# Kernel optimization log

Measured on AMD Instinct MI355X. Metric: run time of the kernel, lower is better.

The kernel has to match this reference:

```python
import jax, jax.numpy as jnp
import numpy as np

N_NODES = 100000
N_EDGES = 1600000
N_GRAPHS = 1000
X_S = 128
HID = 64


def setup_inputs() -> dict:
    key = jax.random.key(0)
    ks = jax.random.split(key, 12)
    x = jax.random.normal(ks[0], (N_NODES, X_S), dtype=jnp.float32)
    edge_index = jax.random.randint(ks[1], (2, N_EDGES), 0, N_NODES, dtype=jnp.int64)
    batch = jnp.sort(jax.random.randint(ks[2], (N_NODES,), 0, N_GRAPHS, dtype=jnp.int64))
    def lin(k, fin, fout):
        s = 1.0 / np.sqrt(fin)
        kw, kb = jax.random.split(k)
        W = jax.random.uniform(kw, (fin, fout), minval=-s, maxval=s, dtype=jnp.float32)
        b = jax.random.uniform(kb, (fout,), minval=-s, maxval=s, dtype=jnp.float32)
        return W, b
    W1, b1 = lin(ks[3], X_S, HID)
    W2, b2 = lin(ks[4], HID, HID)
    W3, b3 = lin(ks[5], HID, HID)
    Wf, bf = lin(ks[6], HID, 10)
    Wl, bl = lin(ks[7], 10, 1)
    eps1 = jnp.float32(0.37)
    eps2 = jnp.float32(0.72)
    eps3 = jnp.float32(0.11)
    return {"x": x, "edge_index": edge_index, "batch": batch,
            "W1": W1, "b1": b1, "W2": W2, "b2": b2, "W3": W3, "b3": b3,
            "Wf": Wf, "bf": bf, "Wl": Wl, "bl": bl,
            "eps1": eps1, "eps2": eps2, "eps3": eps3}


def _gin_conv(h, src, dst, eps, W, b):
    # GIN: nn((1+eps)*x_i + sum_{j in N(i)} x_j); messages flow src -> dst
    agg = jax.ops.segment_sum(h[src], dst, num_segments=N_NODES)  # [N, d]
    return ((1.0 + eps) * h + agg) @ W + b


def reference(x, edge_index, batch, W1, b1, W2, b2, W3, b3, Wf, bf, Wl, bl,
              eps1, eps2, eps3):
    src, dst = edge_index[0], edge_index[1]
    h = jax.nn.relu(_gin_conv(x, src, dst, eps1, W1, b1))
    h = jax.nn.relu(_gin_conv(h, src, dst, eps2, W2, b2))
    h = jax.nn.relu(_gin_conv(h, src, dst, eps3, W3, b3))
    # global_mean_pool over graph ids
    sums = jax.ops.segment_sum(h, batch, num_segments=N_GRAPHS)        # [G, 64]
    cnts = jax.ops.segment_sum(jnp.ones((N_NODES,), h.dtype), batch,
                               num_segments=N_GRAPHS)                   # [G]
    pooled = sums / jnp.maximum(cnts, 1.0)[:, None]
    out = jax.nn.relu(pooled @ Wf + bf) @ Wl + bl                       # [G, 1]
    return out
```

## Files before the change

kernel.cpp:

```cpp
#include <hip/hip_runtime.h>

#define N_NODES 100000
#define N_EDGES 1600000
#define N_GRAPHS 1000

#define NB_C 782
#define B1   256
#define CHUNK (N_EDGES / B1)
#define MTOT (NB_C * B1)

typedef unsigned int uint32;
typedef unsigned short ushort16;
typedef __attribute__((ext_vector_type(8))) short short8;
typedef __attribute__((ext_vector_type(4))) float f32x4;

static __device__ __forceinline__ ushort16 f2bf(float f) {
    uint32 u = __float_as_uint(f);
    u += 0x7fffu + ((u >> 16) & 1u);
    return (ushort16)(u >> 16);
}
static __device__ __forceinline__ uint32 pk2(float a, float b) {
    return (uint32)f2bf(a) | ((uint32)f2bf(b) << 16);
}
static __device__ __forceinline__ void bf2x(uint32 v, float& lo, float& hi) {
    lo = __uint_as_float(v << 16);
    hi = __uint_as_float(v & 0xffff0000u);
}
static __device__ __forceinline__ void acc8(float* a, uint4 v) {
    float lo, hi;
    bf2x(v.x, lo, hi); a[0] += lo; a[1] += hi;
    bf2x(v.y, lo, hi); a[2] += lo; a[3] += hi;
    bf2x(v.z, lo, hi); a[4] += lo; a[5] += hi;
    bf2x(v.w, lo, hi); a[6] += lo; a[7] += hi;
}

union CV8 { uint4 u; short8 s; };

__global__ __launch_bounds__(256) void convw_kernel(
    const float* __restrict__ W1, const float* __restrict__ W2,
    const float* __restrict__ W3,
    ushort16* __restrict__ W1t, ushort16* __restrict__ W2t,
    ushort16* __restrict__ W3t)
{
    int t = threadIdx.x;
    if (blockIdx.x == 0) {
        for (int i = t; i < 64 * 128; i += 256) {
            int j = i >> 7, k = i & 127;
            W1t[i] = f2bf(W1[k * 64 + j]);
        }
    } else if (blockIdx.x == 1) {
        for (int i = t; i < 64 * 64; i += 256) {
            int j = i >> 6, k = i & 63;
            W2t[i] = f2bf(W2[k * 64 + j]);
        }
    } else {
        for (int i = t; i < 64 * 64; i += 256) {
            int j = i >> 6, k = i & 63;
            W3t[i] = f2bf(W3[k * 64 + j]);
        }
    }
}


__global__ __launch_bounds__(256) void count_kernel(
    const int* __restrict__ dst, int* __restrict__ M)
{
    __shared__ int cnt[NB_C];
    int b = blockIdx.x, t = threadIdx.x;
    for (int q = t; q < NB_C; q += 256) cnt[q] = 0;
    __syncthreads();
    int e0 = b * CHUNK;
    for (int e = e0 + t; e < e0 + CHUNK; e += 256)
        atomicAdd(&cnt[dst[e] >> 7], 1);
    __syncthreads();
    for (int q = t; q < NB_C; q += 256) M[q * B1 + b] = cnt[q];
}

#define SCAN_B 1024
#define SCAN_NBLK ((MTOT + SCAN_B - 1) / SCAN_B)

__global__ __launch_bounds__(256) void scanA_kernel(
    const int* __restrict__ in, int* __restrict__ excl, int* __restrict__ bsum)
{
    __shared__ int s[256];
    int b = blockIdx.x, t = threadIdx.x;
    int base = b * SCAN_B + t * 4;
    int v[4];
#pragma unroll
    for (int i = 0; i < 4; ++i) v[i] = (base + i < MTOT) ? in[base + i] : 0;
    int tsum = v[0] + v[1] + v[2] + v[3];
    s[t] = tsum;
    __syncthreads();
    for (int off = 1; off < 256; off <<= 1) {
        int x = (t >= off) ? s[t - off] : 0;
        __syncthreads();
        s[t] += x;
        __syncthreads();
    }
    int run = s[t] - tsum;
#pragma unroll
    for (int i = 0; i < 4; ++i) {
        if (base + i < MTOT) excl[base + i] = run;
        run += v[i];
    }
    if (t == 255) bsum[b] = s[255];
}

__global__ __launch_bounds__(256) void scanB_kernel(int* __restrict__ bsum)
{
    __shared__ int s[256];
    int t = threadIdx.x;
    int v = (t < SCAN_NBLK) ? bsum[t] : 0;
    s[t] = v;
    __syncthreads();
    for (int off = 1; off < 256; off <<= 1) {
        int x = (t >= off) ? s[t - off] : 0;
        __syncthreads();
        s[t] += x;
        __syncthreads();
    }
    if (t < SCAN_NBLK) bsum[t] = s[t] - v;
}

__global__ __launch_bounds__(256) void scanC_kernel(
    const int* __restrict__ excl, const int* __restrict__ bsum,
    int* __restrict__ out)
{
    int b = blockIdx.x, t = threadIdx.x;
    int add = bsum[b];
    int base = b * SCAN_B + t * 4;
#pragma unroll
    for (int i = 0; i < 4; ++i)
        if (base + i < MTOT) out[base + i] = excl[base + i] + add;
}

__global__ __launch_bounds__(256) void scatter_kernel(
    const int* __restrict__ src, const int* __restrict__ dst,
    const int* __restrict__ Ms, uint32* __restrict__ tmp)
{
    __shared__ int cur[NB_C];
    int b = blockIdx.x, t = threadIdx.x;
    for (int q = t; q < NB_C; q += 256) cur[q] = Ms[q * B1 + b];
    __syncthreads();
    int e0 = b * CHUNK;
    for (int e = e0 + t; e < e0 + CHUNK; e += 256) {
        int d = dst[e];
        int q = d >> 7;
        int pos = atomicAdd(&cur[q], 1);
        tmp[pos] = ((uint32)(d & 127) << 17) | (uint32)src[e];
    }
}

__global__ __launch_bounds__(256) void finalize_kernel(
    const uint32* __restrict__ tmp, const int* __restrict__ Ms,
    int* __restrict__ row_off, int* __restrict__ esrc)
{
    __shared__ int cnt[128];
    __shared__ int pref[128];
    __shared__ int cur[128];
    int q = blockIdx.x, t = threadIdx.x;
    int start = Ms[q * B1];
    int end = (q == NB_C - 1) ? N_EDGES : Ms[(q + 1) * B1];

    if (t < 128) cnt[t] = 0;
    __syncthreads();
    for (int e = start + t; e < end; e += 256)
        atomicAdd(&cnt[tmp[e] >> 17], 1);
    __syncthreads();
    if (t < 128) pref[t] = cnt[t];
    __syncthreads();
    for (int off = 1; off < 128; off <<= 1) {
        int x = 0;
        if (t < 128 && t >= off) x = pref[t - off];
        __syncthreads();
        if (t < 128) pref[t] += x;
        __syncthreads();
    }
    if (t < 128) {
        int excl = pref[t] - cnt[t];
        int node = q * 128 + t;
        if (node < N_NODES) row_off[node] = start + excl;
        cur[t] = start + excl;
    }
    if (q == 0 && t == 0) row_off[N_NODES] = N_EDGES;
    __syncthreads();
    for (int e = start + t; e < end; e += 256) {
        uint32 u = tmp[e];
        int pos = atomicAdd(&cur[u >> 17], 1);
        esrc[pos] = (int)(u & 0x1FFFFu);
    }
}

__global__ __launch_bounds__(256) void gemm1_mfma_kernel(
    const float* __restrict__ x,
    const ushort16* __restrict__ Wt,
    ushort16* __restrict__ y)
{
    int lane = threadIdx.x & 63;
    int wave = threadIdx.x >> 6;
    int col = lane & 15, quad = lane >> 4;
    int node0 = blockIdx.x * 64 + wave * 16;
    int anode = node0 + col;

    short8 a[4];
    if (anode < N_NODES) {
        const float* xr = &x[(size_t)anode * 128 + quad * 8];
#pragma unroll
        for (int s = 0; s < 4; ++s) {
            float4 v0 = *(const float4*)&xr[s * 32];
            float4 v1 = *(const float4*)&xr[s * 32 + 4];
            CV8 cv;
            cv.u = make_uint4(pk2(v0.x, v0.y), pk2(v0.z, v0.w),
                              pk2(v1.x, v1.y), pk2(v1.z, v1.w));
            a[s] = cv.s;
        }
    } else {
        short8 z = {0, 0, 0, 0, 0, 0, 0, 0};
#pragma unroll
        for (int s = 0; s < 4; ++s) a[s] = z;
    }

    f32x4 acc[4];
#pragma unroll
    for (int nt = 0; nt < 4; ++nt)
#pragma unroll
        for (int r = 0; r < 4; ++r) acc[nt][r] = 0.0f;

#pragma unroll
    for (int nt = 0; nt < 4; ++nt) {
        const ushort16* wr = &Wt[(size_t)(nt * 16 + col) * 128 + quad * 8];
#pragma unroll
        for (int s = 0; s < 4; ++s) {
            short8 b = *(const short8*)&wr[s * 32];
            acc[nt] = __builtin_amdgcn_mfma_f32_16x16x32_bf16(a[s], b, acc[nt], 0, 0, 0);
        }
    }

#pragma unroll
    for (int nt = 0; nt < 4; ++nt)
#pragma unroll
        for (int r = 0; r < 4; ++r) {
            int node = node0 + quad * 4 + r;
            if (node < N_NODES)
                y[(size_t)node * 64 + nt * 16 + col] = f2bf(acc[nt][r]);
        }
}

__global__ __launch_bounds__(256) void gemm_mfma_kernel(
    const ushort16* __restrict__ hb,
    const ushort16* __restrict__ Wt,
    ushort16* __restrict__ y)
{
    int lane = threadIdx.x & 63;
    int wave = threadIdx.x >> 6;
    int col = lane & 15, quad = lane >> 4;
    int node0 = blockIdx.x * 64 + wave * 16;
    int anode = node0 + col;

    short8 a0, a1;
    if (anode < N_NODES) {
        a0 = *(const short8*)&hb[(size_t)anode * 64 + quad * 8];
        a1 = *(const short8*)&hb[(size_t)anode * 64 + 32 + quad * 8];
    } else {
        short8 z = {0, 0, 0, 0, 0, 0, 0, 0};
        a0 = z; a1 = z;
    }

    f32x4 acc[4];
#pragma unroll
    for (int nt = 0; nt < 4; ++nt)
#pragma unroll
        for (int r = 0; r < 4; ++r) acc[nt][r] = 0.0f;

#pragma unroll
    for (int nt = 0; nt < 4; ++nt) {
        const ushort16* wr = &Wt[(size_t)(nt * 16 + col) * 64 + quad * 8];
        short8 b0 = *(const short8*)&wr[0];
        short8 b1 = *(const short8*)&wr[32];
        acc[nt] = __builtin_amdgcn_mfma_f32_16x16x32_bf16(a0, b0, acc[nt], 0, 0, 0);
        acc[nt] = __builtin_amdgcn_mfma_f32_16x16x32_bf16(a1, b1, acc[nt], 0, 0, 0);
    }

#pragma unroll
    for (int nt = 0; nt < 4; ++nt)
#pragma unroll
        for (int r = 0; r < 4; ++r) {
            int node = node0 + quad * 4 + r;
            if (node < N_NODES)
                y[(size_t)node * 64 + nt * 16 + col] = f2bf(acc[nt][r]);
        }
}

__global__ __launch_bounds__(256) void aggregate_kernel(
    const uint4* __restrict__ y4,
    const int* __restrict__ row_off,
    const int* __restrict__ esrc,
    const float* __restrict__ b,
    const float* __restrict__ eps_p,
    uint4* __restrict__ out4)
{
    int lane = threadIdx.x & 63;
    int wave = threadIdx.x >> 6;
    int grp = lane >> 3;
    int w = lane & 7;
    int node = blockIdx.x * 32 + wave * 8 + grp;

    int s0 = row_off[node], s1 = row_off[node + 1];
    float a[8], c[8];
#pragma unroll
    for (int i = 0; i < 8; ++i) { a[i] = 0.f; c[i] = 0.f; }

    int e = s0;
    for (; e + 3 < s1; e += 4) {
        int i0 = esrc[e];
        int i1 = esrc[e + 1];
        int i2 = esrc[e + 2];
        int i3 = esrc[e + 3];
        uint4 v0 = y4[(size_t)i0 * 8 + w];
        uint4 v1 = y4[(size_t)i1 * 8 + w];
        uint4 v2 = y4[(size_t)i2 * 8 + w];
        uint4 v3 = y4[(size_t)i3 * 8 + w];
        acc8(a, v0);
        acc8(c, v1);
        acc8(a, v2);
        acc8(c, v3);
    }
    for (; e < s1; ++e) {
        int i0 = esrc[e];
        uint4 v0 = y4[(size_t)i0 * 8 + w];
        acc8(a, v0);
    }
#pragma unroll
    for (int i = 0; i < 8; ++i) a[i] += c[i];

    uint4 sv = y4[(size_t)node * 8 + w];
    float s[8];
    bf2x(sv.x, s[0], s[1]);
    bf2x(sv.y, s[2], s[3]);
    bf2x(sv.z, s[4], s[5]);
    bf2x(sv.w, s[6], s[7]);
    float ep1 = 1.0f + eps_p[0];
    float4 b0 = *(const float4*)&b[w * 8];
    float4 b1 = *(const float4*)&b[w * 8 + 4];
    float r0 = fmaxf(fmaf(ep1, s[0], a[0]) + b0.x, 0.0f);
    float r1 = fmaxf(fmaf(ep1, s[1], a[1]) + b0.y, 0.0f);
    float r2 = fmaxf(fmaf(ep1, s[2], a[2]) + b0.z, 0.0f);
    float r3 = fmaxf(fmaf(ep1, s[3], a[3]) + b0.w, 0.0f);
    float r4 = fmaxf(fmaf(ep1, s[4], a[4]) + b1.x, 0.0f);
    float r5 = fmaxf(fmaf(ep1, s[5], a[5]) + b1.y, 0.0f);
    float r6 = fmaxf(fmaf(ep1, s[6], a[6]) + b1.z, 0.0f);
    float r7 = fmaxf(fmaf(ep1, s[7], a[7]) + b1.w, 0.0f);
    out4[(size_t)node * 8 + w] =
        make_uint4(pk2(r0, r1), pk2(r2, r3), pk2(r4, r5), pk2(r6, r7));
}

__global__ __launch_bounds__(256) void pool_head_kernel(
    const uint32* __restrict__ hb,
    const int* __restrict__ batch,
    const float* __restrict__ Wf,
    const float* __restrict__ bfv,
    const float* __restrict__ Wl,
    const float* __restrict__ blv,
    float* __restrict__ out)
{
    __shared__ float red[4][64];
    __shared__ float pooled[64];
    __shared__ float hid[10];
    int g = blockIdx.x;
    int t = threadIdx.x;
    int lo = 0, hi = N_NODES;
    while (lo < hi) { int mid = (lo + hi) >> 1; if (batch[mid] < g) lo = mid + 1; else hi = mid; }
    int start = lo;
    hi = N_NODES;
    while (lo < hi) { int mid = (lo + hi) >> 1; if (batch[mid] < g + 1) lo = mid + 1; else hi = mid; }
    int end = lo;

    int c = t & 63, nl = t >> 6;
    int wd = c >> 1, odd = c & 1;
    float acc = 0.0f;
    for (int i = start + nl; i < end; i += 4) {
        uint32 u = hb[(size_t)i * 32 + wd];
        acc += __uint_as_float(odd ? (u & 0xffff0000u) : (u << 16));
    }
    red[nl][c] = acc;
    __syncthreads();
    if (t < 64) {
        float cnt = (float)(end - start);
        float inv = 1.0f / fmaxf(cnt, 1.0f);
        pooled[t] = (red[0][t] + red[1][t] + red[2][t] + red[3][t]) * inv;
    }
    __syncthreads();
    if (t < 10) {
        float s = bfv[t];
#pragma unroll
        for (int k = 0; k < 64; ++k) s = fmaf(pooled[k], Wf[k * 10 + t], s);
        hid[t] = fmaxf(s, 0.0f);
    }
    __syncthreads();
    if (t == 0) {
        float s = blv[0];
#pragma unroll
        for (int j = 0; j < 10; ++j) s = fmaf(hid[j], Wl[j], s);
        out[g] = s;
    }
}

extern "C" void kernel_launch(void* const* d_in, const int* in_sizes, int n_in,
                              void* d_out, int out_size, void* d_ws, size_t ws_size,
                              hipStream_t stream)
{
    const float* x     = (const float*)d_in[0];
    const int*   ei    = (const int*)  d_in[1];
    const int*   src   = ei;
    const int*   dst   = ei + N_EDGES;
    const int*   batch = (const int*)  d_in[2];
    const float* W1    = (const float*)d_in[3];
    const float* b1    = (const float*)d_in[4];
    const float* W2    = (const float*)d_in[5];
    const float* b2    = (const float*)d_in[6];
    const float* W3    = (const float*)d_in[7];
    const float* b3    = (const float*)d_in[8];
    const float* Wf    = (const float*)d_in[9];
    const float* bfv   = (const float*)d_in[10];
    const float* Wl    = (const float*)d_in[11];
    const float* blv   = (const float*)d_in[12];
    const float* eps1  = (const float*)d_in[13];
    const float* eps2  = (const float*)d_in[14];
    const float* eps3  = (const float*)d_in[15];

    ushort16* ybA = (ushort16*)d_ws;
    ushort16* ybB = ybA + (size_t)N_NODES * 64;
    int*   ints = (int*)(ybB + (size_t)N_NODES * 64);
    int*   M       = ints;
    int*   Mex     = M + MTOT;
    int*   Ms      = Mex + MTOT;
    int*   bsum    = Ms + MTOT;
    int*   row_off = bsum + 256;
    int*   esrc    = row_off + N_NODES + 1;
    uint32* tmp    = (uint32*)(esrc + N_EDGES);
    ushort16* W1t = (ushort16*)(((uintptr_t)(tmp + N_EDGES) + 255) & ~(uintptr_t)255);
    ushort16* W2t = W1t + 64 * 128;
    ushort16* W3t = W2t + 64 * 64;

    const int gemm_blk = (N_NODES + 63) / 64;
    const int agg_blk  = N_NODES / 32;

    convw_kernel<<<3, 256, 0, stream>>>(W1, W2, W3, W1t, W2t, W3t);

    count_kernel<<<B1, 256, 0, stream>>>(dst, M);
    scanA_kernel<<<SCAN_NBLK, 256, 0, stream>>>(M, Mex, bsum);
    scanB_kernel<<<1, 256, 0, stream>>>(bsum);
    scanC_kernel<<<SCAN_NBLK, 256, 0, stream>>>(Mex, bsum, Ms);
    scatter_kernel<<<B1, 256, 0, stream>>>(src, dst, Ms, tmp);
    finalize_kernel<<<NB_C, 256, 0, stream>>>(tmp, Ms, row_off, esrc);

    gemm1_mfma_kernel<<<gemm_blk, 256, 0, stream>>>(x, W1t, ybA);
    aggregate_kernel<<<agg_blk, 256, 0, stream>>>(
        (const uint4*)ybA, row_off, esrc, b1, eps1, (uint4*)ybB);

    gemm_mfma_kernel<<<gemm_blk, 256, 0, stream>>>(ybB, W2t, ybA);
    aggregate_kernel<<<agg_blk, 256, 0, stream>>>(
        (const uint4*)ybA, row_off, esrc, b2, eps2, (uint4*)ybB);

    gemm_mfma_kernel<<<gemm_blk, 256, 0, stream>>>(ybB, W3t, ybA);
    aggregate_kernel<<<agg_blk, 256, 0, stream>>>(
        (const uint4*)ybA, row_off, esrc, b3, eps3, (uint4*)ybB);

    pool_head_kernel<<<N_GRAPHS, 256, 0, stream>>>(
        (const uint32*)ybB, batch, Wf, bfv, Wl, blv, (float*)d_out);
}
```

Measured before the change: 326.1 us.

## Fuse aggregation with GEMM for layers 2-3 and simplify CSR build

For layers 2 and 3 the separate GEMM and aggregate kernels are replaced by one kernel. It first gathers and sums the neighbour features, adds (1+eps) times the node's own features, stages the 16-node tile in LDS, then applies the MFMA GEMM with bias and ReLU. This reverses the original order (transform then aggregate) into aggregate then transform, which gives the same result by linearity, and removes one intermediate write/read round trip per layer plus two launches. The multi-pass bucketed CSR build (count, three-stage scan, scatter, finalize) is replaced by global-atomic degree counting, a single-block scan and a global-atomic scatter, with the counter zeroing folded into the weight-conversion launch. The trade-off is more global atomic contention, a mostly serial single-block scan, and a nondeterministic edge order within each row.

```diff
diff --git a/kernel.cpp b/kernel.cpp
--- a/kernel.cpp
+++ b/kernel.cpp
@@ -4,10 +4,8 @@
 #define N_EDGES 1600000
 #define N_GRAPHS 1000
 
-#define NB_C 782
 #define B1   256
 #define CHUNK (N_EDGES / B1)
-#define MTOT (NB_C * B1)
 
 typedef unsigned int uint32;
 typedef unsigned short ushort16;
@@ -40,154 +38,76 @@
     const float* __restrict__ W1, const float* __restrict__ W2,
     const float* __restrict__ W3,
     ushort16* __restrict__ W1t, ushort16* __restrict__ W2t,
-    ushort16* __restrict__ W3t)
+    ushort16* __restrict__ W3t, int* __restrict__ cnt)
 {
     int t = threadIdx.x;
-    if (blockIdx.x == 0) {
+    int b = blockIdx.x;
+    if (b == 0) {
         for (int i = t; i < 64 * 128; i += 256) {
             int j = i >> 7, k = i & 127;
             W1t[i] = f2bf(W1[k * 64 + j]);
         }
-    } else if (blockIdx.x == 1) {
+    } else if (b == 1) {
         for (int i = t; i < 64 * 64; i += 256) {
             int j = i >> 6, k = i & 63;
             W2t[i] = f2bf(W2[k * 64 + j]);
         }
-    } else {
+    } else if (b == 2) {
         for (int i = t; i < 64 * 64; i += 256) {
             int j = i >> 6, k = i & 63;
             W3t[i] = f2bf(W3[k * 64 + j]);
         }
-    }
-}
-
-
-__global__ __launch_bounds__(256) void count_kernel(
-    const int* __restrict__ dst, int* __restrict__ M)
-{
-    __shared__ int cnt[NB_C];
+    } else {
+        for (int i = (b - 3) * 256 + t; i < N_NODES; i += 98 * 256)
+            cnt[i] = 0;
+    }
+}
+
+__global__ __launch_bounds__(256) void count_glob_kernel(
+    const int* __restrict__ dst, int* __restrict__ cnt)
+{
     int b = blockIdx.x, t = threadIdx.x;
-    for (int q = t; q < NB_C; q += 256) cnt[q] = 0;
-    __syncthreads();
     int e0 = b * CHUNK;
     for (int e = e0 + t; e < e0 + CHUNK; e += 256)
-        atomicAdd(&cnt[dst[e] >> 7], 1);
+        atomicAdd(&cnt[dst[e]], 1);
+}
+
+__global__ __launch_bounds__(1024) void scan_kernel(
+    const int* __restrict__ cnt, int* __restrict__ row_off, int* __restrict__ cur)
+{
+    __shared__ int s[1024];
+    int t = threadIdx.x;
+    const int SEG = (N_NODES + 1023) / 1024;
+    int lo = t * SEG;
+    int hi = lo + SEG; if (hi > N_NODES) hi = N_NODES;
+    int sum = 0;
+    for (int i = lo; i < hi; ++i) sum += cnt[i];
+    s[t] = sum;
     __syncthreads();
-    for (int q = t; q < NB_C; q += 256) M[q * B1 + b] = cnt[q];
-}
-
-#define SCAN_B 1024
-#define SCAN_NBLK ((MTOT + SCAN_B - 1) / SCAN_B)
-
-__global__ __launch_bounds__(256) void scanA_kernel(
-    const int* __restrict__ in, int* __restrict__ excl, int* __restrict__ bsum)
-{
-    __shared__ int s[256];
-    int b = blockIdx.x, t = threadIdx.x;
-    int base = b * SCAN_B + t * 4;
-    int v[4];
-#pragma unroll
-    for (int i = 0; i < 4; ++i) v[i] = (base + i < MTOT) ? in[base + i] : 0;
-    int tsum = v[0] + v[1] + v[2] + v[3];
-    s[t] = tsum;
-    __syncthreads();
-    for (int off = 1; off < 256; off <<= 1) {
+    for (int off = 1; off < 1024; off <<= 1) {
         int x = (t >= off) ? s[t - off] : 0;
         __syncthreads();
         s[t] += x;
         __syncthreads();
     }
-    int run = s[t] - tsum;
-#pragma unroll
-    for (int i = 0; i < 4; ++i) {
-        if (base + i < MTOT) excl[base + i] = run;
-        run += v[i];
-    }
-    if (t == 255) bsum[b] = s[255];
-}
-
-__global__ __launch_bounds__(256) void scanB_kernel(int* __restrict__ bsum)
-{
-    __shared__ int s[256];
-    int t = threadIdx.x;
-    int v = (t < SCAN_NBLK) ? bsum[t] : 0;
-    s[t] = v;
-    __syncthreads();
-    for (int off = 1; off < 256; off <<= 1) {
-        int x = (t >= off) ? s[t - off] : 0;
-        __syncthreads();
-        s[t] += x;
-        __syncthreads();
-    }
-    if (t < SCAN_NBLK) bsum[t] = s[t] - v;
-}
-
-__global__ __launch_bounds__(256) void scanC_kernel(
-    const int* __restrict__ excl, const int* __restrict__ bsum,
-    int* __restrict__ out)
+    int run = s[t] - sum;
+    for (int i = lo; i < hi; ++i) {
+        row_off[i] = run;
+        cur[i] = run;
+        run += cnt[i];
+    }
+    if (t == 0) row_off[N_NODES] = N_EDGES;
+}
+
+__global__ __launch_bounds__(256) void scatter_glob_kernel(
+    const int* __restrict__ src, const int* __restrict__ dst,
+    int* __restrict__ cur, int* __restrict__ esrc)
 {
     int b = blockIdx.x, t = threadIdx.x;
-    int add = bsum[b];
-    int base = b * SCAN_B + t * 4;
-#pragma unroll
-    for (int i = 0; i < 4; ++i)
-        if (base + i < MTOT) out[base + i] = excl[base + i] + add;
-}
-
-__global__ __launch_bounds__(256) void scatter_kernel(
-    const int* __restrict__ src, const int* __restrict__ dst,
-    const int* __restrict__ Ms, uint32* __restrict__ tmp)
-{
-    __shared__ int cur[NB_C];
-    int b = blockIdx.x, t = threadIdx.x;
-    for (int q = t; q < NB_C; q += 256) cur[q] = Ms[q * B1 + b];
-    __syncthreads();
     int e0 = b * CHUNK;
     for (int e = e0 + t; e < e0 + CHUNK; e += 256) {
-        int d = dst[e];
-        int q = d >> 7;
-        int pos = atomicAdd(&cur[q], 1);
-        tmp[pos] = ((uint32)(d & 127) << 17) | (uint32)src[e];
-    }
-}
-
-__global__ __launch_bounds__(256) void finalize_kernel(
-    const uint32* __restrict__ tmp, const int* __restrict__ Ms,
-    int* __restrict__ row_off, int* __restrict__ esrc)
-{
-    __shared__ int cnt[128];
-    __shared__ int pref[128];
-    __shared__ int cur[128];
-    int q = blockIdx.x, t = threadIdx.x;
-    int start = Ms[q * B1];
-    int end = (q == NB_C - 1) ? N_EDGES : Ms[(q + 1) * B1];
-
-    if (t < 128) cnt[t] = 0;
-    __syncthreads();
-    for (int e = start + t; e < end; e += 256)
-        atomicAdd(&cnt[tmp[e] >> 17], 1);
-    __syncthreads();
-    if (t < 128) pref[t] = cnt[t];
-    __syncthreads();
-    for (int off = 1; off < 128; off <<= 1) {
-        int x = 0;
-        if (t < 128 && t >= off) x = pref[t - off];
-        __syncthreads();
-        if (t < 128) pref[t] += x;
-        __syncthreads();
-    }
-    if (t < 128) {
-        int excl = pref[t] - cnt[t];
-        int node = q * 128 + t;
-        if (node < N_NODES) row_off[node] = start + excl;
-        cur[t] = start + excl;
-    }
-    if (q == 0 && t == 0) row_off[N_NODES] = N_EDGES;
-    __syncthreads();
-    for (int e = start + t; e < end; e += 256) {
-        uint32 u = tmp[e];
-        int pos = atomicAdd(&cur[u >> 17], 1);
-        esrc[pos] = (int)(u & 0x1FFFFu);
+        int pos = atomicAdd(&cur[dst[e]], 1);
+        esrc[pos] = src[e];
     }
 }
 
@@ -234,51 +154,6 @@
             short8 b = *(const short8*)&wr[s * 32];
             acc[nt] = __builtin_amdgcn_mfma_f32_16x16x32_bf16(a[s], b, acc[nt], 0, 0, 0);
         }
-    }
-
-#pragma unroll
-    for (int nt = 0; nt < 4; ++nt)
-#pragma unroll
-        for (int r = 0; r < 4; ++r) {
-            int node = node0 + quad * 4 + r;
-            if (node < N_NODES)
-                y[(size_t)node * 64 + nt * 16 + col] = f2bf(acc[nt][r]);
-        }
-}
-
-__global__ __launch_bounds__(256) void gemm_mfma_kernel(
-    const ushort16* __restrict__ hb,
-    const ushort16* __restrict__ Wt,
-    ushort16* __restrict__ y)
-{
-    int lane = threadIdx.x & 63;
-    int wave = threadIdx.x >> 6;
-    int col = lane & 15, quad = lane >> 4;
-    int node0 = blockIdx.x * 64 + wave * 16;
-    int anode = node0 + col;
-
-    short8 a0, a1;
-    if (anode < N_NODES) {
-        a0 = *(const short8*)&hb[(size_t)anode * 64 + quad * 8];
-        a1 = *(const short8*)&hb[(size_t)anode * 64 + 32 + quad * 8];
-    } else {
-        short8 z = {0, 0, 0, 0, 0, 0, 0, 0};
-        a0 = z; a1 = z;
-    }
-
-    f32x4 acc[4];
-#pragma unroll
-    for (int nt = 0; nt < 4; ++nt)
-#pragma unroll
-        for (int r = 0; r < 4; ++r) acc[nt][r] = 0.0f;
-
-#pragma unroll
-    for (int nt = 0; nt < 4; ++nt) {
-        const ushort16* wr = &Wt[(size_t)(nt * 16 + col) * 64 + quad * 8];
-        short8 b0 = *(const short8*)&wr[0];
-        short8 b1 = *(const short8*)&wr[32];
-        acc[nt] = __builtin_amdgcn_mfma_f32_16x16x32_bf16(a0, b0, acc[nt], 0, 0, 0);
-        acc[nt] = __builtin_amdgcn_mfma_f32_16x16x32_bf16(a1, b1, acc[nt], 0, 0, 0);
     }
 
 #pragma unroll
@@ -326,8 +201,7 @@
         acc8(c, v3);
     }
     for (; e < s1; ++e) {
-        int i0 = esrc[e];
-        uint4 v0 = y4[(size_t)i0 * 8 + w];
+        uint4 v0 = y4[(size_t)esrc[e] * 8 + w];
         acc8(a, v0);
     }
 #pragma unroll
@@ -354,6 +228,102 @@
         make_uint4(pk2(r0, r1), pk2(r2, r3), pk2(r4, r5), pk2(r6, r7));
 }
 
+__global__ __launch_bounds__(256) void agg_gemm_fused_kernel(
+    const uint4* __restrict__ h4,
+    const int* __restrict__ row_off,
+    const int* __restrict__ esrc,
+    const ushort16* __restrict__ Wt,
+    const float* __restrict__ bias,
+    const float* __restrict__ eps_p,
+    ushort16* __restrict__ hout)
+{
+    __shared__ __align__(16) ushort16 zl[4][16][72];
+    int lane = threadIdx.x & 63;
+    int wave = threadIdx.x >> 6;
+    int g = lane >> 2;
+    int c = lane & 3;
+    int node0 = blockIdx.x * 64 + wave * 16;
+    if (node0 >= N_NODES) return;
+    int node = node0 + g;
+
+    int s0 = row_off[node], s1 = row_off[node + 1];
+    float a[16], d[16];
+#pragma unroll
+    for (int i = 0; i < 16; ++i) { a[i] = 0.f; d[i] = 0.f; }
+
+    const size_t cb = (size_t)c * 2;
+    int e = s0;
+    for (; e + 3 < s1; e += 4) {
+        int i0 = esrc[e];
+        int i1 = esrc[e + 1];
+        int i2 = esrc[e + 2];
+        int i3 = esrc[e + 3];
+        uint4 v0a = h4[(size_t)i0 * 8 + cb], v0b = h4[(size_t)i0 * 8 + cb + 1];
+        uint4 v1a = h4[(size_t)i1 * 8 + cb], v1b = h4[(size_t)i1 * 8 + cb + 1];
+        uint4 v2a = h4[(size_t)i2 * 8 + cb], v2b = h4[(size_t)i2 * 8 + cb + 1];
+        uint4 v3a = h4[(size_t)i3 * 8 + cb], v3b = h4[(size_t)i3 * 8 + cb + 1];
+        acc8(a, v0a); acc8(a + 8, v0b);
+        acc8(d, v1a); acc8(d + 8, v1b);
+        acc8(a, v2a); acc8(a + 8, v2b);
+        acc8(d, v3a); acc8(d + 8, v3b);
+    }
+    for (; e < s1; ++e) {
+        int i0 = esrc[e];
+        uint4 va = h4[(size_t)i0 * 8 + cb], vb = h4[(size_t)i0 * 8 + cb + 1];
+        acc8(a, va); acc8(a + 8, vb);
+    }
+#pragma unroll
+    for (int i = 0; i < 16; ++i) a[i] += d[i];
+
+    uint4 sva = h4[(size_t)node * 8 + cb], svb = h4[(size_t)node * 8 + cb + 1];
+    float s[16];
+    bf2x(sva.x, s[0], s[1]);  bf2x(sva.y, s[2], s[3]);
+    bf2x(sva.z, s[4], s[5]);  bf2x(sva.w, s[6], s[7]);
+    bf2x(svb.x, s[8], s[9]);  bf2x(svb.y, s[10], s[11]);
+    bf2x(svb.z, s[12], s[13]); bf2x(svb.w, s[14], s[15]);
+    float ep1 = 1.0f + eps_p[0];
+    float z[16];
+#pragma unroll
+    for (int i = 0; i < 16; ++i) z[i] = fmaf(ep1, s[i], a[i]);
+
+    uint4 pA = make_uint4(pk2(z[0], z[1]), pk2(z[2], z[3]),
+                          pk2(z[4], z[5]), pk2(z[6], z[7]));
+    uint4 pB = make_uint4(pk2(z[8], z[9]), pk2(z[10], z[11]),
+                          pk2(z[12], z[13]), pk2(z[14], z[15]));
+    *(uint4*)&zl[wave][g][c * 16] = pA;
+    *(uint4*)&zl[wave][g][c * 16 + 8] = pB;
+
+    int col = lane & 15, quad = lane >> 4;
+    short8 a0 = *(const short8*)&zl[wave][col][quad * 8];
+    short8 a1 = *(const short8*)&zl[wave][col][32 + quad * 8];
+
+    f32x4 acc[4];
+#pragma unroll
+    for (int nt = 0; nt < 4; ++nt)
+#pragma unroll
+        for (int r = 0; r < 4; ++r) acc[nt][r] = 0.0f;
+
+#pragma unroll
+    for (int nt = 0; nt < 4; ++nt) {
+        const ushort16* wr = &Wt[(size_t)(nt * 16 + col) * 64 + quad * 8];
+        short8 b0 = *(const short8*)&wr[0];
+        short8 b1 = *(const short8*)&wr[32];
+        acc[nt] = __builtin_amdgcn_mfma_f32_16x16x32_bf16(a0, b0, acc[nt], 0, 0, 0);
+        acc[nt] = __builtin_amdgcn_mfma_f32_16x16x32_bf16(a1, b1, acc[nt], 0, 0, 0);
+    }
+
+#pragma unroll
+    for (int nt = 0; nt < 4; ++nt) {
+        float bl = bias[nt * 16 + col];
+#pragma unroll
+        for (int r = 0; r < 4; ++r) {
+            int nd = node0 + quad * 4 + r;
+            hout[(size_t)nd * 64 + nt * 16 + col] =
+                f2bf(fmaxf(acc[nt][r] + bl, 0.0f));
+        }
+    }
+}
+
 __global__ __launch_bounds__(256) void pool_head_kernel(
     const uint32* __restrict__ hb,
     const int* __restrict__ batch,
@@ -431,40 +401,33 @@
     ushort16* ybA = (ushort16*)d_ws;
     ushort16* ybB = ybA + (size_t)N_NODES * 64;
     int*   ints = (int*)(ybB + (size_t)N_NODES * 64);
-    int*   M       = ints;
-    int*   Mex     = M + MTOT;
-    int*   Ms      = Mex + MTOT;
-    int*   bsum    = Ms + MTOT;
-    int*   row_off = bsum + 256;
+    int*   cnt     = ints;
+    int*   cur     = cnt + N_NODES;
+    int*   row_off = cur + N_NODES;
     int*   esrc    = row_off + N_NODES + 1;
-    uint32* tmp    = (uint32*)(esrc + N_EDGES);
-    ushort16* W1t = (ushort16*)(((uintptr_t)(tmp + N_EDGES) + 255) & ~(uintptr_t)255);
+    ushort16* W1t = (ushort16*)(((uintptr_t)(esrc + N_EDGES) + 255) & ~(uintptr_t)255);
     ushort16* W2t = W1t + 64 * 128;
     ushort16* W3t = W2t + 64 * 64;
 
-    const int gemm_blk = (N_NODES + 63) / 64;
-    const int agg_blk  = N_NODES / 32;
-
-    convw_kernel<<<3, 256, 0, stream>>>(W1, W2, W3, W1t, W2t, W3t);
-
-    count_kernel<<<B1, 256, 0, stream>>>(dst, M);
-    scanA_kernel<<<SCAN_NBLK, 256, 0, stream>>>(M, Mex, bsum);
-    scanB_kernel<<<1, 256, 0, stream>>>(bsum);
-    scanC_kernel<<<SCAN_NBLK, 256, 0, stream>>>(Mex, bsum, Ms);
-    scatter_kernel<<<B1, 256, 0, stream>>>(src, dst, Ms, tmp);
-    finalize_kernel<<<NB_C, 256, 0, stream>>>(tmp, Ms, row_off, esrc);
+    const int gemm_blk  = (N_NODES + 63) / 64;
+    const int agg_blk   = N_NODES / 32;
+    const int fused_blk = (N_NODES + 63) / 64;
+
+    convw_kernel<<<101, 256, 0, stream>>>(W1, W2, W3, W1t, W2t, W3t, cnt);
+
+    count_glob_kernel<<<B1, 256, 0, stream>>>(dst, cnt);
+    scan_kernel<<<1, 1024, 0, stream>>>(cnt, row_off, cur);
+    scatter_glob_kernel<<<B1, 256, 0, stream>>>(src, dst, cur, esrc);
 
     gemm1_mfma_kernel<<<gemm_blk, 256, 0, stream>>>(x, W1t, ybA);
     aggregate_kernel<<<agg_blk, 256, 0, stream>>>(
         (const uint4*)ybA, row_off, esrc, b1, eps1, (uint4*)ybB);
 
-    gemm_mfma_kernel<<<gemm_blk, 256, 0, stream>>>(ybB, W2t, ybA);
-    aggregate_kernel<<<agg_blk, 256, 0, stream>>>(
-        (const uint4*)ybA, row_off, esrc, b2, eps2, (uint4*)ybB);
-
-    gemm_mfma_kernel<<<gemm_blk, 256, 0, stream>>>(ybB, W3t, ybA);
-    aggregate_kernel<<<agg_blk, 256, 0, stream>>>(
-        (const uint4*)ybA, row_off, esrc, b3, eps3, (uint4*)ybB);
+    agg_gemm_fused_kernel<<<fused_blk, 256, 0, stream>>>(
+        (const uint4*)ybB, row_off, esrc, W2t, b2, eps2, ybA);
+
+    agg_gemm_fused_kernel<<<fused_blk, 256, 0, stream>>>(
+        (const uint4*)ybA, row_off, esrc, W3t, b3, eps3, ybB);
 
     pool_head_kernel<<<N_GRAPHS, 256, 0, stream>>>(
         (const uint32*)ybB, batch, Wf, bfv, Wl, blv, (float*)d_out);
```

New measurement: 629.4 us. 1.93x slower.

## Fuse neighbor aggregation with following MFMA GEMM for GIN layers two and three

Applied to the files above, without the earlier changes.

Layers 2 and 3 now aggregate the neighbours first and apply the linear layer second, inside one kernel. Each wave gathers and sums neighbour features for 16 nodes and adds the (1+eps) self term. It stages the combined rows in LDS as bf16, runs the 64x64 MFMA, and applies bias and ReLU. This removes two separate GEMM launches and the round trip of their intermediate bf16 activations through global memory. The cost is that each lane now gathers 16 features instead of 8, which may reduce memory-level parallelism. The pre-GEMM sum is also rounded to bf16, a small precision change.

```diff
diff --git a/kernel.cpp b/kernel.cpp
--- a/kernel.cpp
+++ b/kernel.cpp
@@ -234,51 +234,6 @@
             short8 b = *(const short8*)&wr[s * 32];
             acc[nt] = __builtin_amdgcn_mfma_f32_16x16x32_bf16(a[s], b, acc[nt], 0, 0, 0);
         }
-    }
-
-#pragma unroll
-    for (int nt = 0; nt < 4; ++nt)
-#pragma unroll
-        for (int r = 0; r < 4; ++r) {
-            int node = node0 + quad * 4 + r;
-            if (node < N_NODES)
-                y[(size_t)node * 64 + nt * 16 + col] = f2bf(acc[nt][r]);
-        }
-}
-
-__global__ __launch_bounds__(256) void gemm_mfma_kernel(
-    const ushort16* __restrict__ hb,
-    const ushort16* __restrict__ Wt,
-    ushort16* __restrict__ y)
-{
-    int lane = threadIdx.x & 63;
-    int wave = threadIdx.x >> 6;
-    int col = lane & 15, quad = lane >> 4;
-    int node0 = blockIdx.x * 64 + wave * 16;
-    int anode = node0 + col;
-
-    short8 a0, a1;
-    if (anode < N_NODES) {
-        a0 = *(const short8*)&hb[(size_t)anode * 64 + quad * 8];
-        a1 = *(const short8*)&hb[(size_t)anode * 64 + 32 + quad * 8];
-    } else {
-        short8 z = {0, 0, 0, 0, 0, 0, 0, 0};
-        a0 = z; a1 = z;
-    }
-
-    f32x4 acc[4];
-#pragma unroll
-    for (int nt = 0; nt < 4; ++nt)
-#pragma unroll
-        for (int r = 0; r < 4; ++r) acc[nt][r] = 0.0f;
-
-#pragma unroll
-    for (int nt = 0; nt < 4; ++nt) {
-        const ushort16* wr = &Wt[(size_t)(nt * 16 + col) * 64 + quad * 8];
-        short8 b0 = *(const short8*)&wr[0];
-        short8 b1 = *(const short8*)&wr[32];
-        acc[nt] = __builtin_amdgcn_mfma_f32_16x16x32_bf16(a0, b0, acc[nt], 0, 0, 0);
-        acc[nt] = __builtin_amdgcn_mfma_f32_16x16x32_bf16(a1, b1, acc[nt], 0, 0, 0);
     }
 
 #pragma unroll
@@ -326,8 +281,7 @@
         acc8(c, v3);
     }
     for (; e < s1; ++e) {
-        int i0 = esrc[e];
-        uint4 v0 = y4[(size_t)i0 * 8 + w];
+        uint4 v0 = y4[(size_t)esrc[e] * 8 + w];
         acc8(a, v0);
     }
 #pragma unroll
@@ -354,6 +308,102 @@
         make_uint4(pk2(r0, r1), pk2(r2, r3), pk2(r4, r5), pk2(r6, r7));
 }
 
+__global__ __launch_bounds__(256) void agg_gemm_fused_kernel(
+    const uint4* __restrict__ h4,
+    const int* __restrict__ row_off,
+    const int* __restrict__ esrc,
+    const ushort16* __restrict__ Wt,
+    const float* __restrict__ bias,
+    const float* __restrict__ eps_p,
+    ushort16* __restrict__ hout)
+{
+    __shared__ __align__(16) ushort16 zl[4][16][72];
+    int lane = threadIdx.x & 63;
+    int wave = threadIdx.x >> 6;
+    int g = lane >> 2;
+    int c = lane & 3;
+    int node0 = blockIdx.x * 64 + wave * 16;
+    if (node0 >= N_NODES) return;
+    int node = node0 + g;
+
+    int s0 = row_off[node], s1 = row_off[node + 1];
+    float a[16], d[16];
+#pragma unroll
+    for (int i = 0; i < 16; ++i) { a[i] = 0.f; d[i] = 0.f; }
+
+    const size_t cb = (size_t)c * 2;
+    int e = s0;
+    for (; e + 3 < s1; e += 4) {
+        int i0 = esrc[e];
+        int i1 = esrc[e + 1];
+        int i2 = esrc[e + 2];
+        int i3 = esrc[e + 3];
+        uint4 v0a = h4[(size_t)i0 * 8 + cb], v0b = h4[(size_t)i0 * 8 + cb + 1];
+        uint4 v1a = h4[(size_t)i1 * 8 + cb], v1b = h4[(size_t)i1 * 8 + cb + 1];
+        uint4 v2a = h4[(size_t)i2 * 8 + cb], v2b = h4[(size_t)i2 * 8 + cb + 1];
+        uint4 v3a = h4[(size_t)i3 * 8 + cb], v3b = h4[(size_t)i3 * 8 + cb + 1];
+        acc8(a, v0a); acc8(a + 8, v0b);
+        acc8(d, v1a); acc8(d + 8, v1b);
+        acc8(a, v2a); acc8(a + 8, v2b);
+        acc8(d, v3a); acc8(d + 8, v3b);
+    }
+    for (; e < s1; ++e) {
+        int i0 = esrc[e];
+        uint4 va = h4[(size_t)i0 * 8 + cb], vb = h4[(size_t)i0 * 8 + cb + 1];
+        acc8(a, va); acc8(a + 8, vb);
+    }
+#pragma unroll
+    for (int i = 0; i < 16; ++i) a[i] += d[i];
+
+    uint4 sva = h4[(size_t)node * 8 + cb], svb = h4[(size_t)node * 8 + cb + 1];
+    float s[16];
+    bf2x(sva.x, s[0], s[1]);  bf2x(sva.y, s[2], s[3]);
+    bf2x(sva.z, s[4], s[5]);  bf2x(sva.w, s[6], s[7]);
+    bf2x(svb.x, s[8], s[9]);  bf2x(svb.y, s[10], s[11]);
+    bf2x(svb.z, s[12], s[13]); bf2x(svb.w, s[14], s[15]);
+    float ep1 = 1.0f + eps_p[0];
+    float z[16];
+#pragma unroll
+    for (int i = 0; i < 16; ++i) z[i] = fmaf(ep1, s[i], a[i]);
+
+    uint4 pA = make_uint4(pk2(z[0], z[1]), pk2(z[2], z[3]),
+                          pk2(z[4], z[5]), pk2(z[6], z[7]));
+    uint4 pB = make_uint4(pk2(z[8], z[9]), pk2(z[10], z[11]),
+                          pk2(z[12], z[13]), pk2(z[14], z[15]));
+    *(uint4*)&zl[wave][g][c * 16] = pA;
+    *(uint4*)&zl[wave][g][c * 16 + 8] = pB;
+
+    int col = lane & 15, quad = lane >> 4;
+    short8 a0 = *(const short8*)&zl[wave][col][quad * 8];
+    short8 a1 = *(const short8*)&zl[wave][col][32 + quad * 8];
+
+    f32x4 acc[4];
+#pragma unroll
+    for (int nt = 0; nt < 4; ++nt)
+#pragma unroll
+        for (int r = 0; r < 4; ++r) acc[nt][r] = 0.0f;
+
+#pragma unroll
+    for (int nt = 0; nt < 4; ++nt) {
+        const ushort16* wr = &Wt[(size_t)(nt * 16 + col) * 64 + quad * 8];
+        short8 b0 = *(const short8*)&wr[0];
+        short8 b1 = *(const short8*)&wr[32];
+        acc[nt] = __builtin_amdgcn_mfma_f32_16x16x32_bf16(a0, b0, acc[nt], 0, 0, 0);
+        acc[nt] = __builtin_amdgcn_mfma_f32_16x16x32_bf16(a1, b1, acc[nt], 0, 0, 0);
+    }
+
+#pragma unroll
+    for (int nt = 0; nt < 4; ++nt) {
+        float bl = bias[nt * 16 + col];
+#pragma unroll
+        for (int r = 0; r < 4; ++r) {
+            int nd = node0 + quad * 4 + r;
+            hout[(size_t)nd * 64 + nt * 16 + col] =
+                f2bf(fmaxf(acc[nt][r] + bl, 0.0f));
+        }
+    }
+}
+
 __global__ __launch_bounds__(256) void pool_head_kernel(
     const uint32* __restrict__ hb,
     const int* __restrict__ batch,
@@ -442,8 +492,9 @@
     ushort16* W2t = W1t + 64 * 128;
     ushort16* W3t = W2t + 64 * 64;
 
-    const int gemm_blk = (N_NODES + 63) / 64;
-    const int agg_blk  = N_NODES / 32;
+    const int gemm_blk  = (N_NODES + 63) / 64;
+    const int agg_blk   = N_NODES / 32;
+    const int fused_blk = (N_NODES + 63) / 64;
 
     convw_kernel<<<3, 256, 0, stream>>>(W1, W2, W3, W1t, W2t, W3t);
 
@@ -458,13 +509,11 @@
     aggregate_kernel<<<agg_blk, 256, 0, stream>>>(
         (const uint4*)ybA, row_off, esrc, b1, eps1, (uint4*)ybB);
 
-    gemm_mfma_kernel<<<gemm_blk, 256, 0, stream>>>(ybB, W2t, ybA);
-    aggregate_kernel<<<agg_blk, 256, 0, stream>>>(
-        (const uint4*)ybA, row_off, esrc, b2, eps2, (uint4*)ybB);
-
-    gemm_mfma_kernel<<<gemm_blk, 256, 0, stream>>>(ybB, W3t, ybA);
-    aggregate_kernel<<<agg_blk, 256, 0, stream>>>(
-        (const uint4*)ybA, row_off, esrc, b3, eps3, (uint4*)ybB);
+    agg_gemm_fused_kernel<<<fused_blk, 256, 0, stream>>>(
+        (const uint4*)ybB, row_off, esrc, W2t, b2, eps2, ybA);
+
+    agg_gemm_fused_kernel<<<fused_blk, 256, 0, stream>>>(
+        (const uint4*)ybA, row_off, esrc, W3t, b3, eps3, ybB);
 
     pool_head_kernel<<<N_GRAPHS, 256, 0, stream>>>(
         (const uint32*)ybB, batch, Wf, bfv, Wl, blv, (float*)d_out);
```

Result: faster. 312.3 us (-4.2%).
